# Kernel optimization log

Hardware: AMD Instinct MI355X
Metric: run time of the kernel (lower is better)

Reference implementation:

```python
import math
import jax, jax.numpy as jnp
import numpy as np

N_FEATURES = 32
DEGREE = 3
BATCH = 8192
N_POLY = math.comb(N_FEATURES + DEGREE, DEGREE)  # 6545


def _build_monomial_indices(n_features, degree):
    """Static (numpy) indices replicating the Pascal-triangle recursion in TaylorMap._poly.

    For degree level i (i = 1..degree-1), the original code appends, for each feature f,
    x[:, f] * prev_block[:, :comb(i+f, i)].  We flatten that into gather index arrays so the
    whole block is one vectorized gather+multiply instead of a Python loop of slices/concats.
    """
    levels = []
    for i in range(1, degree):
        counts = np.array([math.comb(i + f, i) for f in range(n_features)], dtype=np.int64)
        f_idx = np.repeat(np.arange(n_features, dtype=np.int64), counts)
        m_idx = np.concatenate([np.arange(c, dtype=np.int64) for c in counts])
        levels.append((f_idx, m_idx))
    return levels

_LEVELS = _build_monomial_indices(N_FEATURES, DEGREE)


def _poly(x):
    # x: [B, n].  Returns [B, n_poly] monomial features in the exact order of TaylorMap._poly.
    b = x.shape[0]
    parts = [jnp.ones((b, 1), x.dtype), x]
    prev = x
    for f_idx, m_idx in _LEVELS:  # static loop over degree levels (degree-1 iterations)
        new = x[:, f_idx] * prev[:, m_idx]  # [B, comb(n+i, i+1)-ish block]
        parts.append(new)
        prev = new
    return jnp.concatenate(parts, axis=-1)


def setup_inputs() -> dict:
    key = jax.random.key(0)
    kx, kw = jax.random.split(key)
    x = jax.random.normal(kx, (BATCH, N_FEATURES), dtype=jnp.float32)
    # learned weight W: [n_poly, n_features] (default init is zeros; use small randn for a
    # non-degenerate numerical baseline)
    W = jax.random.normal(kw, (N_POLY, N_FEATURES), dtype=jnp.float32) * 0.02
    return {"x": x, "W": W}


def reference(x, W):
    # TaylorMap(x) = x * residual + poly(x) @ W   (residual=True)
    return x + _poly(x) @ W
```

## Files before the change

### kernel.cpp

```cpp
#include <hip/hip_runtime.h>
#include <cstdint>
#include <cstddef>
#include <utility>


#define NF 32
#define NPOLY 6545
#define NSTEPS 417
#define NOCT 834
#define NDESC 842
#define TSTRIDE 576
#define D2OFF 40
#define XDSTRIDE 34

#define T_BYTES   36864
#define XD_OFF    36864
#define XD_BYTES  2176
#define DESC_OFF  39040
#define DESC_BYTES 3368
#define SMEM_BYTES 42496

typedef _Float16 f16x8 __attribute__((ext_vector_type(8)));
typedef float f32x16 __attribute__((ext_vector_type(16)));

#define D2N 528
struct D2I { uint8_t a[D2N]; uint8_t b[D2N]; };
constexpr D2I build_d2i() {
    D2I t{};
    int k = 0;
    for (int f = 0; f < NF; ++f)
        for (int m = 0; m <= f; ++m) { t.a[k] = (uint8_t)f; t.b[k] = (uint8_t)m; ++k; }
    return t;
}
constexpr D2I D2T = build_d2i();

struct Desc { uint32_t d[NOCT]; };
constexpr Desc build_desc() {
    Desc D{};
    int u = 0;
    for (int o = 0; o < 72; ++o)
        D.d[u++] = (uint32_t)(o * 16);
    for (int f = 0; f < NF; ++f) {
        int cnt = (f + 1) * (f + 2) / 2;
        for (int j8 = 0; j8 < (cnt + 7) / 8; ++j8)
            D.d[u++] = (uint32_t)((D2OFF + 8 * j8) * 2) | ((uint32_t)((1 + f) * 2) << 16);
    }
    return D;
}
__device__ const Desc DESC_G = build_desc();

struct Oldk { int16_t v[NSTEPS * 16]; };
constexpr Oldk build_oldk() {
    Oldk K{};
    int k = 0;
    for (int ti = 0; ti < 576; ++ti) {
        int old;
        if (ti == 0) old = 0;
        else if (ti <= 32) old = ti;
        else if (ti >= D2OFF && ti < D2OFF + D2N) old = 33 + (ti - D2OFF);
        else old = -1;
        K.v[k++] = (int16_t)old;
    }
    for (int f = 0; f < NF; ++f) {
        int cnt = (f + 1) * (f + 2) / 2;
        int off3 = 0;
        for (int g = 0; g < f; ++g) off3 += (g + 1) * (g + 2) / 2;
        int oc = (cnt + 7) / 8;
        for (int m = 0; m < oc * 8; ++m)
            K.v[k++] = (int16_t)(m < cnt ? 561 + off3 + m : -1);
    }
    return K;
}
__device__ const Oldk OLDK_G = build_oldk();

template<int TI>
__device__ __forceinline__ _Float16 tval(const float (&xr)[NF]) {
    if constexpr (TI == 0) return (_Float16)1.0f;
    else if constexpr (TI >= 1 && TI <= 32) return (_Float16)xr[TI - 1];
    else if constexpr (TI >= D2OFF && TI < D2OFF + D2N) {
        constexpr int m = TI - D2OFF;
        return (_Float16)(xr[D2T.a[m]] * xr[D2T.b[m]]);
    } else return (_Float16)0.0f;
}

template<int O, int... Js>
__device__ __forceinline__ void put_oct(std::integer_sequence<int, Js...>,
                                        const float (&xr)[NF], _Float16* trow, int r) {
    f16x8 v = { tval<O * 8 + Js>(xr)... };
    int slot = (O & ~7) | ((O ^ r) & 7);
    *(f16x8*)(trow + slot * 8) = v;
}

template<int BASE, int... Os>
__device__ __forceinline__ void p1_octs(std::integer_sequence<int, Os...>,
                                        const float (&xr)[NF], _Float16* trow, int r) {
    (put_oct<BASE + Os>(std::make_integer_sequence<int, 8>{}, xr, trow, r), ...);
}

template<int V>
__device__ __forceinline__ void xdw(const float (&xr)[NF], _Float16* xdrow) {
    if constexpr (V == 0) xdrow[0] = (_Float16)1.0f;
    else if constexpr (V <= 32) xdrow[V] = (_Float16)xr[V - 1];
}

template<int G>
__device__ __forceinline__ void p1_group(const float (&xr)[NF], _Float16* trow,
                                         _Float16* xdrow, int r) {
    if constexpr (G < 8)
        p1_octs<G * 5>(std::make_integer_sequence<int, 5>{}, xr, trow, r);
    else
        p1_octs<40 + (G - 8) * 4>(std::make_integer_sequence<int, 4>{}, xr, trow, r);
    xdw<2 * G>(xr, xdrow);
    xdw<2 * G + 1>(xr, xdrow);
    if constexpr (G == 15) xdw<32>(xr, xdrow);
}

__global__ void prep(const float* __restrict__ W, _Float16* __restrict__ Wh) {
    int id = blockIdx.x * 256 + threadIdx.x;
    if (id < NSTEPS * 64) {
        int step = id >> 6, rem = id & 63, hs = rem >> 5, n = rem & 31;
        int k0 = step * 16 + hs * 8;
        f16x8 v;
#pragma unroll
        for (int j = 0; j < 8; ++j) {
            int old = OLDK_G.v[k0 + j];
            v[j] = (_Float16)(old >= 0 ? W[old * 32 + n] : 0.0f);
        }
        *(f16x8*)(Wh + (size_t)id * 8) = v;
    }
}

__global__ __launch_bounds__(512, 2) void gemm(const float* __restrict__ x,
                                               const _Float16* __restrict__ Wh,
                                               float* __restrict__ out) {
    __shared__ __align__(16) unsigned char smem[SMEM_BYTES];
    _Float16* t  = (_Float16*)smem;
    _Float16* xd = (_Float16*)(smem + XD_OFF);
    uint32_t* descL = (uint32_t*)(smem + DESC_OFF);

    const int tid = threadIdx.x;
    const int wave = __builtin_amdgcn_readfirstlane(tid >> 6);
    const int lane = tid & 63;
    const int hsel = lane >> 5, r = lane & 31;
    const int mtile = blockIdx.x;

    {
        const int pr = tid & 31, g = tid >> 5;
        float xr[NF];
        const float4* xp = (const float4*)(x + (size_t)(mtile * 32 + pr) * NF);
#pragma unroll
        for (int i = 0; i < 8; ++i) {
            float4 v = xp[i];
            xr[4 * i + 0] = v.x; xr[4 * i + 1] = v.y;
            xr[4 * i + 2] = v.z; xr[4 * i + 3] = v.w;
        }
        _Float16* trow = t + pr * TSTRIDE;
        _Float16* xdrow = xd + pr * XDSTRIDE;
        switch (g) {
            case  0: p1_group< 0>(xr, trow, xdrow, pr); break;
            case  1: p1_group< 1>(xr, trow, xdrow, pr); break;
            case  2: p1_group< 2>(xr, trow, xdrow, pr); break;
            case  3: p1_group< 3>(xr, trow, xdrow, pr); break;
            case  4: p1_group< 4>(xr, trow, xdrow, pr); break;
            case  5: p1_group< 5>(xr, trow, xdrow, pr); break;
            case  6: p1_group< 6>(xr, trow, xdrow, pr); break;
            case  7: p1_group< 7>(xr, trow, xdrow, pr); break;
            case  8: p1_group< 8>(xr, trow, xdrow, pr); break;
            case  9: p1_group< 9>(xr, trow, xdrow, pr); break;
            case 10: p1_group<10>(xr, trow, xdrow, pr); break;
            case 11: p1_group<11>(xr, trow, xdrow, pr); break;
            case 12: p1_group<12>(xr, trow, xdrow, pr); break;
            case 13: p1_group<13>(xr, trow, xdrow, pr); break;
            case 14: p1_group<14>(xr, trow, xdrow, pr); break;
            default: p1_group<15>(xr, trow, xdrow, pr); break;
        }
#pragma unroll
        for (int i = tid; i < NDESC; i += 512)
            descL[i] = (i < NOCT) ? DESC_G.d[i] : 0u;
    }
    __syncthreads();

    const int s0 = __builtin_amdgcn_readfirstlane((wave * NSTEPS) >> 3);
    const int s1 = __builtin_amdgcn_readfirstlane(((wave + 1) * NSTEPS) >> 3);
    const char* trowB = (const char*)t + r * (TSTRIDE * 2);
    const char* xdrowB = (const char*)xd + r * (XDSTRIDE * 2);
    const char* wpB = (const char*)Wh + lane * 16;
    const uint32_t rx = (uint32_t)((r & 7) << 4);

    f32x16 acc0, acc1;
#pragma unroll
    for (int i = 0; i < 16; ++i) { acc0[i] = 0.0f; acc1[i] = 0.0f; }

    uint32_t dva = descL[2 * s0 + hsel];
    uint32_t dvb = descL[2 * s0 + 2 + hsel];
    f16x8 araw0 = *(const f16x8*)(trowB + ((dva & 0xffffu) ^ rx));
    _Float16 xs0 = *(const _Float16*)(xdrowB + (dva >> 16));
    f16x8 araw1 = *(const f16x8*)(trowB + ((dvb & 0xffffu) ^ rx));
    _Float16 xs1 = *(const _Float16*)(xdrowB + (dvb >> 16));
    uint32_t dval0 = descL[2 * (s0 + 2) + hsel];
    uint32_t dval1 = descL[2 * (s0 + 3) + hsel];
    f16x8 breg0 = *(const f16x8*)(wpB + (size_t)s0 * 1024);
    f16x8 breg1 = *(const f16x8*)(wpB + (size_t)(s0 + 1) * 1024);

#define BODY(P, SCUR) do {                                                    \
    uint32_t d_ = dval##P;                                                    \
    f16x8 xsv_ = { xs##P, xs##P, xs##P, xs##P, xs##P, xs##P, xs##P, xs##P };  \
    f16x8 a_ = araw##P * xsv_;                                                \
    f16x8 bu_ = breg##P;                                                      \
    araw##P = *(const f16x8*)(trowB + ((d_ & 0xffffu) ^ rx));                 \
    xs##P   = *(const _Float16*)(xdrowB + (d_ >> 16));                        \
    dval##P = descL[2 * ((SCUR) + 4) + hsel];                                 \
    breg##P = *(const f16x8*)(wpB + (size_t)((SCUR) + 2) * 1024);             \
    acc##P = __builtin_amdgcn_mfma_f32_32x32x16_f16(a_, bu_, acc##P, 0, 0, 0);\
} while (0)

    int s = s0;
    for (; s + 1 < s1; s += 2) { BODY(0, s); BODY(1, s + 1); }
    if (s < s1) {
        f16x8 xsv_ = { xs0, xs0, xs0, xs0, xs0, xs0, xs0, xs0 };
        f16x8 a_ = araw0 * xsv_;
        acc0 = __builtin_amdgcn_mfma_f32_32x32x16_f16(a_, breg0, acc0, 0, 0, 0);
    }
#undef BODY

    __syncthreads();
    float* red = (float*)smem;
    float* bank = red + wave * 1024;
#pragma unroll
    for (int reg = 0; reg < 16; ++reg) {
        int rr = (reg & 3) + 8 * (reg >> 2) + 4 * hsel;
        bank[rr * 32 + r] = acc0[reg] + acc1[reg];
    }
    __syncthreads();
    const float* xg = x + (size_t)mtile * 1024;
    float* op = out + (size_t)mtile * 1024;
#pragma unroll
    for (int i = 0; i < 2; ++i) {
        int e = tid + i * 512;
        float v = red[e] + red[1024 + e] + red[2048 + e] + red[3072 + e]
                + red[4096 + e] + red[5120 + e] + red[6144 + e] + red[7168 + e];
        op[e] = xg[e] + v;
    }
}

extern "C" void kernel_launch(void* const* d_in, const int* in_sizes, int n_in,
                              void* d_out, int out_size, void* d_ws, size_t ws_size,
                              hipStream_t stream) {
    (void)in_sizes; (void)n_in; (void)out_size; (void)ws_size;
    const float* x = (const float*)d_in[0];
    const float* W = (const float*)d_in[1];
    float* out = (float*)d_out;
    _Float16* Wh = (_Float16*)d_ws;

    prep<<<105, 256, 0, stream>>>(W, Wh);
    gemm<<<256, 512, 0, stream>>>(x, Wh, out);
}
```

Before: 71.00 us.

## Split K across two blocks per M tile with atomic accumulation and register descriptors

Each 32-row M tile is now processed by two blocks that each take half of the K steps, doubling the grid to 512 blocks. Partial results are combined with atomicAdd into an output that the prep kernel pre-initialises with x. Step descriptors are no longer staged in shared memory; each wave loads its slice into registers once and pulls entries with readlane. The aim is more parallelism and a smaller LDS footprint. The cost is that each block recomputes the monomial tile, the result depends on atomic ordering, and the readlane index assumes a wave covers at most 64 descriptor pairs.

```diff
diff --git a/kernel.cpp b/kernel.cpp
--- a/kernel.cpp
+++ b/kernel.cpp
@@ -8,17 +8,14 @@
 #define NPOLY 6545
 #define NSTEPS 417
 #define NOCT 834
-#define NDESC 842
+#define NDESC 1024
 #define TSTRIDE 576
 #define D2OFF 40
 #define XDSTRIDE 34
 
 #define T_BYTES   36864
 #define XD_OFF    36864
-#define XD_BYTES  2176
-#define DESC_OFF  39040
-#define DESC_BYTES 3368
-#define SMEM_BYTES 42496
+#define SMEM_BYTES 39040
 
 typedef _Float16 f16x8 __attribute__((ext_vector_type(8)));
 typedef float f32x16 __attribute__((ext_vector_type(16)));
@@ -34,7 +31,7 @@
 }
 constexpr D2I D2T = build_d2i();
 
-struct Desc { uint32_t d[NOCT]; };
+struct Desc { uint32_t d[NDESC]; };
 constexpr Desc build_desc() {
     Desc D{};
     int u = 0;
@@ -45,6 +42,7 @@
         for (int j8 = 0; j8 < (cnt + 7) / 8; ++j8)
             D.d[u++] = (uint32_t)((D2OFF + 8 * j8) * 2) | ((uint32_t)((1 + f) * 2) << 16);
     }
+    while (u < NDESC) D.d[u++] = 0u;
     return D;
 }
 __device__ const Desc DESC_G = build_desc();
@@ -115,18 +113,25 @@
     if constexpr (G == 15) xdw<32>(xr, xdrow);
 }
 
-__global__ void prep(const float* __restrict__ W, _Float16* __restrict__ Wh) {
-    int id = blockIdx.x * 256 + threadIdx.x;
-    if (id < NSTEPS * 64) {
-        int step = id >> 6, rem = id & 63, hs = rem >> 5, n = rem & 31;
-        int k0 = step * 16 + hs * 8;
-        f16x8 v;
-#pragma unroll
-        for (int j = 0; j < 8; ++j) {
-            int old = OLDK_G.v[k0 + j];
-            v[j] = (_Float16)(old >= 0 ? W[old * 32 + n] : 0.0f);
+__global__ void prep(const float* __restrict__ x, const float* __restrict__ W,
+                     float* __restrict__ out, _Float16* __restrict__ Wh) {
+    int b = blockIdx.x;
+    if (b < 256) {
+        int id = b * 256 + threadIdx.x;
+        ((float4*)out)[id] = ((const float4*)x)[id];
+    } else {
+        int id = (b - 256) * 256 + threadIdx.x;
+        if (id < NSTEPS * 64) {
+            int step = id >> 6, rem = id & 63, hs = rem >> 5, n = rem & 31;
+            int k0 = step * 16 + hs * 8;
+            f16x8 v;
+#pragma unroll
+            for (int j = 0; j < 8; ++j) {
+                int old = OLDK_G.v[k0 + j];
+                v[j] = (_Float16)(old >= 0 ? W[old * 32 + n] : 0.0f);
+            }
+            *(f16x8*)(Wh + (size_t)id * 8) = v;
         }
-        *(f16x8*)(Wh + (size_t)id * 8) = v;
     }
 }
 
@@ -136,13 +141,13 @@
     __shared__ __align__(16) unsigned char smem[SMEM_BYTES];
     _Float16* t  = (_Float16*)smem;
     _Float16* xd = (_Float16*)(smem + XD_OFF);
-    uint32_t* descL = (uint32_t*)(smem + DESC_OFF);
 
     const int tid = threadIdx.x;
     const int wave = __builtin_amdgcn_readfirstlane(tid >> 6);
     const int lane = tid & 63;
     const int hsel = lane >> 5, r = lane & 31;
-    const int mtile = blockIdx.x;
+    const int mtile = blockIdx.x >> 1;
+    const int kh = blockIdx.x & 1;
 
     {
         const int pr = tid & 31, g = tid >> 5;
@@ -174,14 +179,17 @@
             case 14: p1_group<14>(xr, trow, xdrow, pr); break;
             default: p1_group<15>(xr, trow, xdrow, pr); break;
         }
-#pragma unroll
-        for (int i = tid; i < NDESC; i += 512)
-            descL[i] = (i < NOCT) ? DESC_G.d[i] : 0u;
-    }
+    }
+
+    const int c = kh * 8 + wave;
+    const int s0 = __builtin_amdgcn_readfirstlane((c * NSTEPS) >> 4);
+    const int s1 = __builtin_amdgcn_readfirstlane(((c + 1) * NSTEPS) >> 4);
+    int didx = 2 * (s0 + lane);
+    uint32_t vD0 = DESC_G.d[didx];
+    uint32_t vD1 = DESC_G.d[didx + 1];
+
     __syncthreads();
 
-    const int s0 = __builtin_amdgcn_readfirstlane((wave * NSTEPS) >> 3);
-    const int s1 = __builtin_amdgcn_readfirstlane(((wave + 1) * NSTEPS) >> 3);
     const char* trowB = (const char*)t + r * (TSTRIDE * 2);
     const char* xdrowB = (const char*)xd + r * (XDSTRIDE * 2);
     const char* wpB = (const char*)Wh + lane * 16;
@@ -191,25 +199,25 @@
 #pragma unroll
     for (int i = 0; i < 16; ++i) { acc0[i] = 0.0f; acc1[i] = 0.0f; }
 
-    uint32_t dva = descL[2 * s0 + hsel];
-    uint32_t dvb = descL[2 * s0 + 2 + hsel];
-    f16x8 araw0 = *(const f16x8*)(trowB + ((dva & 0xffffu) ^ rx));
-    _Float16 xs0 = *(const _Float16*)(xdrowB + (dva >> 16));
-    f16x8 araw1 = *(const f16x8*)(trowB + ((dvb & 0xffffu) ^ rx));
-    _Float16 xs1 = *(const _Float16*)(xdrowB + (dvb >> 16));
-    uint32_t dval0 = descL[2 * (s0 + 2) + hsel];
-    uint32_t dval1 = descL[2 * (s0 + 3) + hsel];
+#define DSEL(IDX) (hsel ? __builtin_amdgcn_readlane(vD1, (IDX)) \
+                        : __builtin_amdgcn_readlane(vD0, (IDX)))
+
+    uint32_t dp0 = DSEL(0);
+    uint32_t dp1 = DSEL(1);
+    f16x8 araw0 = *(const f16x8*)(trowB + ((dp0 & 0xffffu) ^ rx));
+    _Float16 xs0 = *(const _Float16*)(xdrowB + (dp0 >> 16));
+    f16x8 araw1 = *(const f16x8*)(trowB + ((dp1 & 0xffffu) ^ rx));
+    _Float16 xs1 = *(const _Float16*)(xdrowB + (dp1 >> 16));
     f16x8 breg0 = *(const f16x8*)(wpB + (size_t)s0 * 1024);
     f16x8 breg1 = *(const f16x8*)(wpB + (size_t)(s0 + 1) * 1024);
 
 #define BODY(P, SCUR) do {                                                    \
-    uint32_t d_ = dval##P;                                                    \
     f16x8 xsv_ = { xs##P, xs##P, xs##P, xs##P, xs##P, xs##P, xs##P, xs##P };  \
     f16x8 a_ = araw##P * xsv_;                                                \
     f16x8 bu_ = breg##P;                                                      \
-    araw##P = *(const f16x8*)(trowB + ((d_ & 0xffffu) ^ rx));                 \
-    xs##P   = *(const _Float16*)(xdrowB + (d_ >> 16));                        \
-    dval##P = descL[2 * ((SCUR) + 4) + hsel];                                 \
+    uint32_t dn_ = DSEL((SCUR) + 2 - s0);                                     \
+    araw##P = *(const f16x8*)(trowB + ((dn_ & 0xffffu) ^ rx));                \
+    xs##P   = *(const _Float16*)(xdrowB + (dn_ >> 16));                       \
     breg##P = *(const f16x8*)(wpB + (size_t)((SCUR) + 2) * 1024);             \
     acc##P = __builtin_amdgcn_mfma_f32_32x32x16_f16(a_, bu_, acc##P, 0, 0, 0);\
 } while (0)
@@ -222,6 +230,7 @@
         acc0 = __builtin_amdgcn_mfma_f32_32x32x16_f16(a_, breg0, acc0, 0, 0, 0);
     }
 #undef BODY
+#undef DSEL
 
     __syncthreads();
     float* red = (float*)smem;
@@ -232,14 +241,13 @@
         bank[rr * 32 + r] = acc0[reg] + acc1[reg];
     }
     __syncthreads();
-    const float* xg = x + (size_t)mtile * 1024;
     float* op = out + (size_t)mtile * 1024;
 #pragma unroll
     for (int i = 0; i < 2; ++i) {
         int e = tid + i * 512;
         float v = red[e] + red[1024 + e] + red[2048 + e] + red[3072 + e]
                 + red[4096 + e] + red[5120 + e] + red[6144 + e] + red[7168 + e];
-        op[e] = xg[e] + v;
+        atomicAdd(op + e, v);
     }
 }
 
@@ -252,6 +260,6 @@
     float* out = (float*)d_out;
     _Float16* Wh = (_Float16*)d_ws;
 
-    prep<<<105, 256, 0, stream>>>(W, Wh);
-    gemm<<<256, 512, 0, stream>>>(x, Wh, out);
-}
+    prep<<<361, 256, 0, stream>>>(x, W, out, Wh);
+    gemm<<<512, 512, 0, stream>>>(x, Wh, out);
+}
```

After: 69.97 us. Within noise of the previous version (-1.4%).
